# Kernel optimization log

Hardware: AMD Instinct MI355X
Metric: run time of the kernel (lower is better)

## Reference

```python
import jax, jax.numpy as jnp
import numpy as np

N = 50000
E = 800000
IN_C = 128
OUT_C = 128
N_TYPES = 3
NEG_SLOPE = 0.2  # PyG GATConv default negative_slope


def setup_inputs() -> dict:
    key = jax.random.key(0)
    ks = jax.random.split(key, 10)
    x = jax.random.normal(ks[0], (N, IN_C), dtype=jnp.float32)
    edge_index = jax.random.randint(ks[1], (2, E), 0, N, dtype=jnp.int32)
    edge_type = jax.random.randint(ks[2], (E,), 0, N_TYPES, dtype=jnp.int32)
    node_type = jax.random.randint(ks[3], (N,), 0, 3, dtype=jnp.int32)
    s = 1.0 / np.sqrt(IN_C)
    emb_table = jax.random.normal(ks[4], (3, IN_C), dtype=jnp.float32)
    W = jax.random.normal(ks[5], (N_TYPES, IN_C, OUT_C), dtype=jnp.float32) * s
    att_src = jax.random.normal(ks[6], (N_TYPES, OUT_C), dtype=jnp.float32) * s
    att_dst = jax.random.normal(ks[7], (N_TYPES, OUT_C), dtype=jnp.float32) * s
    bias = jax.random.normal(ks[8], (N_TYPES, OUT_C), dtype=jnp.float32) * 0.01
    return {"x": x, "edge_index": edge_index, "edge_type": edge_type,
            "node_type": node_type, "emb_table": emb_table, "W": W,
            "att_src": att_src, "att_dst": att_dst, "bias": bias}


def reference(x, edge_index, edge_type, node_type, emb_table, W, att_src, att_dst, bias):
    # Eval mode: dropouts are identity. edge_index is non-empty -> GAT branch.
    n = x.shape[0]
    x = x + emb_table[node_type]  # node-type embedding add
    src, dst = edge_index[0], edge_index[1]
    out_sum = jnp.zeros((n, OUT_C), dtype=x.dtype)
    for t in range(N_TYPES):  # per-edge-type GATConv (heads=1, add_self_loops=True)
        xw = x @ W[t]                       # [N, out]
        a_s = xw @ att_src[t]               # [N] alpha_src per node
        a_d = xw @ att_dst[t]               # [N] alpha_dst per node
        mask = edge_type == t               # [E]
        e_raw = jax.nn.leaky_relu(a_s[src] + a_d[dst], NEG_SLOPE)  # [E]
        e_self = jax.nn.leaky_relu(a_s + a_d, NEG_SLOPE)           # [N] self-loop logit
        e_masked = jnp.where(mask, e_raw, -jnp.inf)
        m = jnp.maximum(jax.ops.segment_max(e_masked, dst, num_segments=n), e_self)
        m = jax.lax.stop_gradient(m)
        w_edge = jnp.where(mask, jnp.exp(e_raw - m[dst]), 0.0)     # [E]
        w_self = jnp.exp(e_self - m)                               # [N]
        denom = jax.ops.segment_sum(w_edge, dst, num_segments=n) + w_self
        num = jax.ops.segment_sum(w_edge[:, None] * xw[src], dst, num_segments=n) \
              + w_self[:, None] * xw
        out_sum = out_sum + num / denom[:, None] + bias[t]
        # (attention weights per type are w_edge/denom[dst]; only node output returned)
    return out_sum
```

## Files before the change

### kernel.cpp

```cpp
#include <hip/hip_runtime.h>
#include <math.h>

#define N_NODES 50000
#define N_EDGES 800000
#define C 128
#define NT 3
#define NEG 0.2f
#define CAP 64

#define GEMM_XB 782

typedef __attribute__((ext_vector_type(8))) short short8;
typedef __attribute__((ext_vector_type(4))) float f32x4;

__device__ __forceinline__ float leaky(float v) { return v > 0.f ? v : NEG * v; }

__device__ __forceinline__ unsigned short f2bf(float f) {
  unsigned int u = __float_as_uint(f);
  u = (u + 0x7FFFu + ((u >> 16) & 1u)) >> 16;
  return (unsigned short)u;
}
__device__ __forceinline__ float bf_lo(unsigned int w) { return __uint_as_float(w << 16); }
__device__ __forceinline__ float bf_hi(unsigned int w) { return __uint_as_float(w & 0xFFFF0000u); }

__global__ void k_prep(const float* __restrict__ W, unsigned short* __restrict__ Wt,
                       int* __restrict__ cnt) {
  int bid = blockIdx.x;
  if (bid < 192) {
    int idx = bid * 256 + threadIdx.x;
    int t = idx >> 14, rem = idx & 16383;
    int n = rem >> 7, k = rem & 127;
    Wt[((size_t)t * C + n) * C + k] = f2bf(W[((size_t)t * C + k) * C + n]);
  } else {
    int i4 = (bid - 192) * 256 + threadIdx.x;
    if (i4 < N_NODES / 4) ((int4*)cnt)[i4] = make_int4(0, 0, 0, 0);
  }
}

__global__ void k_main(const float* __restrict__ x, const int* __restrict__ node_type,
                       const float* __restrict__ emb, const unsigned short* __restrict__ Wt,
                       unsigned short* __restrict__ xwb,
                       const float* __restrict__ att_src, const float* __restrict__ att_dst,
                       float* __restrict__ a_s, float2* __restrict__ ad_es,
                       const int* __restrict__ ei, const int* __restrict__ etype,
                       int* __restrict__ cnt, int* __restrict__ buckets) {
  __shared__ unsigned short As[64][136];
  __shared__ unsigned short Bs[128][136];
  const int bid = blockIdx.x;
  const int tid = threadIdx.x;

  if (bid & 1) {
    int e0 = ((bid >> 1) * 256 + tid) * 4;
    if (e0 + 4 <= N_EDGES) {
      int4 s4 = *(const int4*)(ei + e0);
      int4 d4 = *(const int4*)(ei + N_EDGES + e0);
      int4 t4 = *(const int4*)(etype + e0);
      int p0 = atomicAdd(&cnt[d4.x], 1);
      int p1 = atomicAdd(&cnt[d4.y], 1);
      int p2 = atomicAdd(&cnt[d4.z], 1);
      int p3 = atomicAdd(&cnt[d4.w], 1);
      if (p0 < CAP) buckets[(size_t)d4.x * CAP + p0] = t4.x * N_NODES + s4.x;
      if (p1 < CAP) buckets[(size_t)d4.y * CAP + p1] = t4.y * N_NODES + s4.y;
      if (p2 < CAP) buckets[(size_t)d4.z * CAP + p2] = t4.z * N_NODES + s4.z;
      if (p3 < CAP) buckets[(size_t)d4.w * CAP + p3] = t4.w * N_NODES + s4.w;
    }
    return;
  }

  const int wid = tid >> 6, lane = tid & 63;
  const int m = lane & 15, quad = lane >> 4;
  const int row0 = (bid >> 1) * 64;

#pragma unroll
  for (int it = 0; it < 8; ++it) {
    int c = tid + it * 256;
    int rr = c >> 5, q = c & 31;
    int row = row0 + rr;
    float4 xv = make_float4(0.f, 0.f, 0.f, 0.f);
    int nt = 0;
    if (row < N_NODES) {
      xv = *(const float4*)(x + (size_t)row * C + q * 4);
      nt = node_type[row];
    }
    float4 ev = ((const float4*)emb)[nt * 32 + q];
    ushort4 o;
    o.x = f2bf(xv.x + ev.x); o.y = f2bf(xv.y + ev.y);
    o.z = f2bf(xv.z + ev.z); o.w = f2bf(xv.w + ev.w);
    *(ushort4*)&As[rr][q * 4] = o;
  }
#pragma unroll
  for (int it = 0; it < 8; ++it) {
    int c = tid + it * 256;
    int n = c >> 4, kc = c & 15;
    *(uint4*)&Bs[n][kc * 8] = *(const uint4*)(Wt + (size_t)n * C + kc * 8);
  }
  __syncthreads();

  for (int t = 0; t < NT; ++t) {
    f32x4 acc[8] = {};
#pragma unroll
    for (int k0 = 0; k0 < 128; k0 += 32) {
      short8 a = *(const short8*)&As[wid * 16 + m][k0 + quad * 8];
#pragma unroll
      for (int j = 0; j < 8; ++j) {
        short8 b = *(const short8*)&Bs[j * 16 + m][k0 + quad * 8];
        acc[j] = __builtin_amdgcn_mfma_f32_16x16x32_bf16(a, b, acc[j], 0, 0, 0);
      }
    }

    float ps[4] = {}, pd[4] = {};
#pragma unroll
    for (int j = 0; j < 8; ++j) {
      float as = att_src[t * C + j * 16 + m];
      float ad = att_dst[t * C + j * 16 + m];
#pragma unroll
      for (int reg = 0; reg < 4; ++reg) {
        int row = row0 + wid * 16 + quad * 4 + reg;
        float v = acc[j][reg];
        if (row < N_NODES) xwb[((size_t)t * N_NODES + row) * C + j * 16 + m] = f2bf(v);
        ps[reg] += v * as;
        pd[reg] += v * ad;
      }
    }
#pragma unroll
    for (int off = 1; off < 16; off <<= 1) {
#pragma unroll
      for (int reg = 0; reg < 4; ++reg) {
        ps[reg] += __shfl_xor(ps[reg], off);
        pd[reg] += __shfl_xor(pd[reg], off);
      }
    }
    if (m == 0) {
#pragma unroll
      for (int reg = 0; reg < 4; ++reg) {
        int row = row0 + wid * 16 + quad * 4 + reg;
        if (row < N_NODES) {
          int idx = t * N_NODES + row;
          a_s[idx] = ps[reg];
          ad_es[idx] = make_float2(pd[reg], leaky(ps[reg] + pd[reg]));
        }
      }
    }

    if (t + 1 < NT) {
      __syncthreads();
      const unsigned short* Wtt = Wt + (size_t)(t + 1) * C * C;
#pragma unroll
      for (int it = 0; it < 8; ++it) {
        int c = tid + it * 256;
        int n = c >> 4, kc = c & 15;
        *(uint4*)&Bs[n][kc * 8] = *(const uint4*)(Wtt + (size_t)n * C + kc * 8);
      }
      __syncthreads();
    }
  }
}

__global__ void k_gather(const int* __restrict__ cnt, const int* __restrict__ buckets,
                         const unsigned short* __restrict__ xwb,
                         const float* __restrict__ a_s, const float2* __restrict__ ad_es,
                         const float* __restrict__ bias, float* __restrict__ out) {
  __shared__ float wcs[4][64];
  int wid = threadIdx.x >> 6;
  int lane = threadIdx.x & 63;
  int i = blockIdx.x * 4 + wid;
  int iu = __builtin_amdgcn_readfirstlane(i);
  const int* __restrict__ brow = buckets + (size_t)iu * CAP;
  int n = cnt[iu];
  if (n > CAP) n = CAP;

  int idxl = 0;
  if (lane < n) idxl = brow[lane];
  int tl = idxl >= 2 * N_NODES ? 2 : (idxl >= N_NODES ? 1 : 0);
  float as = a_s[idxl];
  float2 am = ad_es[tl * N_NODES + iu];
  float wl = (lane < n) ? __expf(leaky(as + am.x) - am.y) : 0.f;

  float s0 = tl == 0 ? wl : 0.f;
  float s1 = tl == 1 ? wl : 0.f;
  float s2 = tl == 2 ? wl : 0.f;
#pragma unroll
  for (int off = 1; off < 64; off <<= 1) {
    s0 += __shfl_xor(s0, off);
    s1 += __shfl_xor(s1, off);
    s2 += __shfl_xor(s2, off);
  }
  float inv3[NT] = {1.f / (s0 + 1.f), 1.f / (s1 + 1.f), 1.f / (s2 + 1.f)};
  wcs[wid][lane] = wl * inv3[tl];

  float acc0 = 0.f, acc1 = 0.f;
#pragma unroll
  for (int t = 0; t < NT; ++t) {
    int idx = t * N_NODES + iu;
    float coef = inv3[t];
    unsigned int w = ((const unsigned int*)(xwb + (size_t)idx * C))[lane];
    float2 b2 = ((const float2*)(bias + t * C))[lane];
    acc0 += coef * bf_lo(w) + b2.x;
    acc1 += coef * bf_hi(w) + b2.y;
  }

  const unsigned int* xwu = (const unsigned int*)xwb;
  int j = 0;
  for (; j + 16 <= n; j += 16) {
    float ac0 = 0.f, ac1 = 0.f;
#pragma unroll
    for (int k = 0; k < 16; ++k) {
      int idx = brow[j + k];
      float c = wcs[wid][j + k];
      unsigned int v = xwu[(size_t)idx * (C / 2) + lane];
      ac0 += c * bf_lo(v);
      ac1 += c * bf_hi(v);
    }
    acc0 += ac0; acc1 += ac1;
  }
  for (; j + 8 <= n; j += 8) {
    float ac0 = 0.f, ac1 = 0.f;
#pragma unroll
    for (int k = 0; k < 8; ++k) {
      int idx = brow[j + k];
      float c = wcs[wid][j + k];
      unsigned int v = xwu[(size_t)idx * (C / 2) + lane];
      ac0 += c * bf_lo(v);
      ac1 += c * bf_hi(v);
    }
    acc0 += ac0; acc1 += ac1;
  }
  for (; j < n; ++j) {
    int idx = brow[j];
    float c = wcs[wid][j];
    unsigned int v = xwu[(size_t)idx * (C / 2) + lane];
    acc0 += c * bf_lo(v);
    acc1 += c * bf_hi(v);
  }
  ((float2*)(out + (size_t)iu * C))[lane] = make_float2(acc0, acc1);
}

extern "C" void kernel_launch(void* const* d_in, const int* in_sizes, int n_in,
                              void* d_out, int out_size, void* d_ws, size_t ws_size,
                              hipStream_t stream) {
  const float* x       = (const float*)d_in[0];
  const int* edge_idx  = (const int*)d_in[1];
  const int* edge_type = (const int*)d_in[2];
  const int* node_type = (const int*)d_in[3];
  const float* emb     = (const float*)d_in[4];
  const float* W       = (const float*)d_in[5];
  const float* att_src = (const float*)d_in[6];
  const float* att_dst = (const float*)d_in[7];
  const float* bias    = (const float*)d_in[8];
  float* out = (float*)d_out;

  unsigned short* xwb = (unsigned short*)d_ws;
  unsigned short* Wt  = xwb + (size_t)NT * N_NODES * C;
  float*  a_s   = (float*)(Wt + (size_t)NT * C * C);
  float2* ad_es = (float2*)(a_s + (size_t)NT * N_NODES);
  int*    cnt   = (int*)(ad_es + (size_t)NT * N_NODES);
  int*    buckets = (int*)(cnt + N_NODES);

  k_prep<<<192 + 49, 256, 0, stream>>>(W, Wt, cnt);

  k_main<<<2 * GEMM_XB, 256, 0, stream>>>(x, node_type, emb, Wt, xwb, att_src, att_dst,
                                          a_s, ad_es, edge_idx, edge_type, cnt, buckets);

  k_gather<<<N_NODES / 4, 256, 0, stream>>>(cnt, buckets, xwb, a_s, ad_es, bias, out);
}
```

Before: 189.1 us.

## Load GEMM operands directly into registers, dropping LDS staging and barriers

The GEMM part of k_main stops staging the x+embedding tile and the transposed weights in shared memory. Each lane now builds its A fragments in registers straight from global memory and reads B fragments for every MFMA directly from global (L1/L2-cached) weights. This removes 52KB of LDS per block and all __syncthreads, which can raise occupancy and let the GEMM blocks overlap better with the atomic bucketing blocks. The cost is that every wave re-fetches the full weight matrix per type from cache instead of sharing one LDS copy, so global/L2 traffic goes up.

New measurement: 226.1 us. 1.2x slower.

```diff
diff --git a/kernel.cpp b/kernel.cpp
--- a/kernel.cpp
+++ b/kernel.cpp
@@ -44,8 +44,6 @@
                        float* __restrict__ a_s, float2* __restrict__ ad_es,
                        const int* __restrict__ ei, const int* __restrict__ etype,
                        int* __restrict__ cnt, int* __restrict__ buckets) {
-  __shared__ unsigned short As[64][136];
-  __shared__ unsigned short Bs[128][136];
   const int bid = blockIdx.x;
   const int tid = threadIdx.x;
 
@@ -71,40 +69,44 @@
   const int m = lane & 15, quad = lane >> 4;
   const int row0 = (bid >> 1) * 64;
 
-#pragma unroll
-  for (int it = 0; it < 8; ++it) {
-    int c = tid + it * 256;
-    int rr = c >> 5, q = c & 31;
-    int row = row0 + rr;
-    float4 xv = make_float4(0.f, 0.f, 0.f, 0.f);
-    int nt = 0;
-    if (row < N_NODES) {
-      xv = *(const float4*)(x + (size_t)row * C + q * 4);
-      nt = node_type[row];
-    }
-    float4 ev = ((const float4*)emb)[nt * 32 + q];
-    ushort4 o;
-    o.x = f2bf(xv.x + ev.x); o.y = f2bf(xv.y + ev.y);
-    o.z = f2bf(xv.z + ev.z); o.w = f2bf(xv.w + ev.w);
-    *(ushort4*)&As[rr][q * 4] = o;
-  }
-#pragma unroll
-  for (int it = 0; it < 8; ++it) {
-    int c = tid + it * 256;
-    int n = c >> 4, kc = c & 15;
-    *(uint4*)&Bs[n][kc * 8] = *(const uint4*)(Wt + (size_t)n * C + kc * 8);
-  }
-  __syncthreads();
+  short8 af[4];
+  {
+    int arow = row0 + wid * 16 + m;
+    bool valid = arow < N_NODES;
+    const float* xr = x + (size_t)(valid ? arow : 0) * C;
+    int nt = valid ? node_type[arow] : 0;
+    const float* er = emb + nt * C;
+#pragma unroll
+    for (int k0i = 0; k0i < 4; ++k0i) {
+      int cb = k0i * 32 + quad * 8;
+      float4 v0 = *(const float4*)(xr + cb);
+      float4 v1 = *(const float4*)(xr + cb + 4);
+      float4 e0 = *(const float4*)(er + cb);
+      float4 e1 = *(const float4*)(er + cb + 4);
+      short8 f;
+      f[0] = (short)f2bf(v0.x + e0.x);
+      f[1] = (short)f2bf(v0.y + e0.y);
+      f[2] = (short)f2bf(v0.z + e0.z);
+      f[3] = (short)f2bf(v0.w + e0.w);
+      f[4] = (short)f2bf(v1.x + e1.x);
+      f[5] = (short)f2bf(v1.y + e1.y);
+      f[6] = (short)f2bf(v1.z + e1.z);
+      f[7] = (short)f2bf(v1.w + e1.w);
+      af[k0i] = f;
+    }
+  }
 
   for (int t = 0; t < NT; ++t) {
+    const unsigned short* Wtt = Wt + (size_t)t * C * C;
     f32x4 acc[8] = {};
 #pragma unroll
-    for (int k0 = 0; k0 < 128; k0 += 32) {
-      short8 a = *(const short8*)&As[wid * 16 + m][k0 + quad * 8];
+    for (int k0i = 0; k0i < 4; ++k0i) {
+      int co = k0i * 32 + quad * 8;
+      const unsigned short* bp = Wtt + (size_t)m * C + co;
 #pragma unroll
       for (int j = 0; j < 8; ++j) {
-        short8 b = *(const short8*)&Bs[j * 16 + m][k0 + quad * 8];
-        acc[j] = __builtin_amdgcn_mfma_f32_16x16x32_bf16(a, b, acc[j], 0, 0, 0);
+        short8 b = *(const short8*)(bp + (size_t)j * 16 * C);
+        acc[j] = __builtin_amdgcn_mfma_f32_16x16x32_bf16(af[k0i], b, acc[j], 0, 0, 0);
       }
     }
 
@@ -140,18 +142,6 @@
           ad_es[idx] = make_float2(pd[reg], leaky(ps[reg] + pd[reg]));
         }
       }
-    }
-
-    if (t + 1 < NT) {
-      __syncthreads();
-      const unsigned short* Wtt = Wt + (size_t)(t + 1) * C * C;
-#pragma unroll
-      for (int it = 0; it < 8; ++it) {
-        int c = tid + it * 256;
-        int n = c >> 4, kc = c & 15;
-        *(uint4*)&Bs[n][kc * 8] = *(const uint4*)(Wtt + (size_t)n * C + kc * 8);
-      }
-      __syncthreads();
     }
   }
 }
```
